# Kernel optimization log

Measured on AMD Instinct MI355X. Metric: run time of the kernel, lower is better.

The kernel has to match this reference:

```python
import jax, jax.numpy as jnp
import numpy as np

N_EMBD = 1024
N_HEAD = 16
HEAD_DIM = N_EMBD // N_HEAD


def setup_inputs() -> dict:
    key = jax.random.key(0)
    ks = jax.random.split(key, 9)
    B, T, C = 2, 2048, N_EMBD
    s = 1.0 / np.sqrt(C)
    x = jax.random.normal(ks[0], (B, T, C), dtype=jnp.float32)
    Wk = jax.random.normal(ks[1], (C, C), dtype=jnp.float32) * s
    bk = jnp.zeros((C,), dtype=jnp.float32)
    Wq = jax.random.normal(ks[2], (C, C), dtype=jnp.float32) * s
    bq = jnp.zeros((C,), dtype=jnp.float32)
    Wv = jax.random.normal(ks[3], (C, C), dtype=jnp.float32) * s
    bv = jnp.zeros((C,), dtype=jnp.float32)
    Wp = jax.random.normal(ks[4], (C, C), dtype=jnp.float32) * s
    bp = jnp.zeros((C,), dtype=jnp.float32)
    return {"x": x, "Wk": Wk, "bk": bk, "Wq": Wq, "bq": bq,
            "Wv": Wv, "bv": bv, "Wp": Wp, "bp": bp}


def reference(x, Wk, bk, Wq, bq, Wv, bv, Wp, bp):
    B, T, C = x.shape
    H, D = N_HEAD, HEAD_DIM
    # torch Linear: y = x @ W.T + b
    k = (x @ Wk.T + bk).reshape(B, T, H, D)  # [B,T,H,D]
    q = (x @ Wq.T + bq).reshape(B, T, H, D)
    v = (x @ Wv.T + bv).reshape(B, T, H, D)
    scale = 1.0 / jnp.sqrt(jnp.asarray(D, dtype=x.dtype))
    scores = jnp.einsum('bqhd,bkhd->bhqk', q, k) * scale  # [B,H,T,T]
    w = jax.nn.softmax(scores, axis=-1)
    attn = jnp.einsum('bhqk,bkhd->bqhd', w, v).reshape(B, T, C)
    return attn @ Wp.T + bp
```

## Files before the change

### kernel.cpp

```cpp
#include <hip/hip_runtime.h>
#include <hip/hip_bf16.h>
#include <stdint.h>

#define TT 2048
#define CC 1024
#define NH 16
#define HD 64
#define QKVN 3072

typedef __attribute__((ext_vector_type(8))) short short8;
typedef __attribute__((ext_vector_type(4))) float floatx4;
typedef __attribute__((ext_vector_type(4))) unsigned short ushortx4;

typedef const __attribute__((address_space(1))) void gas_void;
typedef __attribute__((address_space(3))) void las_void;

__device__ __forceinline__ void gload16(const void* g, void* l) {
  __builtin_amdgcn_global_load_lds((gas_void*)g, (las_void*)l, 16, 0, 0);
}

__device__ __forceinline__ unsigned short f2bf(float f) {
  union { float f; uint32_t u; } v; v.f = f;
  uint32_t u = v.u;
  uint32_t r = (u + 0x7fffu + ((u >> 16) & 1u)) >> 16;
  return (unsigned short)r;
}

__device__ __forceinline__ float fexp2(float x) {
#if __has_builtin(__builtin_amdgcn_exp2f)
  return __builtin_amdgcn_exp2f(x);
#else
  return exp2f(x);
#endif
}

#define QSCALE 0.18033688011112042f

__device__ __forceinline__ int perm64(int t) {
  const int kk = t >> 5, r5 = t & 31;
  const int g = ((r5 >> 3) & 2) | ((r5 >> 2) & 1);
  const int slot = (r5 & 3) | ((r5 >> 1) & 4);
  return kk * 32 + g * 8 + slot;
}

__global__ __launch_bounds__(256) void cvt_fused(const float* __restrict__ x,
                                                 const float* __restrict__ wq,
                                                 const float* __restrict__ wk,
                                                 const float* __restrict__ wv,
                                                 const float* __restrict__ wp,
                                                 unsigned short* __restrict__ xb,
                                                 unsigned short* __restrict__ wqkvb,
                                                 unsigned short* __restrict__ wpb) {
  const int i = blockIdx.x * blockDim.x + threadIdx.x;
  if (i < 1048576) {
    const float4 v = reinterpret_cast<const float4*>(x)[i];
    ushortx4 o; o[0] = f2bf(v.x); o[1] = f2bf(v.y); o[2] = f2bf(v.z); o[3] = f2bf(v.w);
    reinterpret_cast<ushortx4*>(xb)[i] = o;
    return;
  }
  const int j = i - 1048576;
  const int seg = j >> 18;
  const int idx = j & 262143;
  const float* src = (seg == 0) ? wq : (seg == 1) ? wk : (seg == 2) ? wv : wp;
  const float sc = (seg == 0) ? QSCALE : 1.0f;
  const float4 v = reinterpret_cast<const float4*>(src)[idx];
  ushortx4 o;
  o[0] = f2bf(v.x * sc); o[1] = f2bf(v.y * sc); o[2] = f2bf(v.z * sc); o[3] = f2bf(v.w * sc);
  if (seg < 3)
    reinterpret_cast<ushortx4*>(wqkvb)[j] = o;
  else
    reinterpret_cast<ushortx4*>(wpb)[idx] = o;
}

template<int OUTF32, int VOUT>
__global__ __launch_bounds__(256) void gemm_bt(const unsigned short* __restrict__ A,
                                               const unsigned short* __restrict__ W,
                                               const float* __restrict__ b0,
                                               const float* __restrict__ b1,
                                               const float* __restrict__ b2,
                                               float bs0,
                                               void* __restrict__ outv,
                                               unsigned short* __restrict__ Vt,
                                               int M, int N, int K) {
  __shared__ unsigned short lsA[128 * 64];
  __shared__ unsigned short lsB[128 * 64];
  const int tid = threadIdx.x;
  const int wave = tid >> 6, lane = tid & 63;
  const int m0 = blockIdx.y * 128, n0 = blockIdx.x * 128;
  const int wm = (wave >> 1) * 64, wn = (wave & 1) * 64;
  const float* bias = (n0 < 1024) ? b0 : (n0 < 2048 ? b1 : b2);
  const float bsc = (n0 < 1024) ? bs0 : 1.0f;

  floatx4 acc[4][4];
#pragma unroll
  for (int i = 0; i < 4; ++i)
#pragma unroll
    for (int j = 0; j < 4; ++j)
      acc[i][j] = (floatx4){0.f, 0.f, 0.f, 0.f};

  const int sr = lane >> 3;
  const int sj = lane & 7;

  for (int kt = 0; kt < K; kt += 64) {
    __syncthreads();
#pragma unroll
    for (int t = 0; t < 4; ++t) {
      const int g4 = wave * 4 + t;
      const int r = g4 * 8 + sr;
      const int gj = (sj ^ (r & 7)) << 3;
      gload16(A + (size_t)(m0 + r) * K + kt + gj, (char*)lsA + g4 * 1024);
      gload16(W + (size_t)(n0 + r) * K + kt + gj, (char*)lsB + g4 * 1024);
    }
    __syncthreads();

#pragma unroll
    for (int kk = 0; kk < 2; ++kk) {
      short8 af[4], bfr[4];
#pragma unroll
      for (int i = 0; i < 4; ++i) {
        const int ra = wm + i * 16 + (lane & 15);
        const int ca = (kk * 4 + (lane >> 4)) ^ (ra & 7);
        af[i] = *reinterpret_cast<const short8*>((const char*)lsA + ra * 128 + (ca << 4));
        const int rb = wn + i * 16 + (lane & 15);
        const int cb = (kk * 4 + (lane >> 4)) ^ (rb & 7);
        bfr[i] = *reinterpret_cast<const short8*>((const char*)lsB + rb * 128 + (cb << 4));
      }
#pragma unroll
      for (int i = 0; i < 4; ++i)
#pragma unroll
        for (int j = 0; j < 4; ++j)
          acc[i][j] = __builtin_amdgcn_mfma_f32_16x16x32_bf16(af[i], bfr[j], acc[i][j], 0, 0, 0);
    }
  }

  const int col = lane & 15;
  const int rgrp = (lane >> 4) * 4;

  if (VOUT && n0 >= 2048) {
#pragma unroll
    for (int i = 0; i < 4; ++i) {
      const int tk0 = m0 + wm + i * 16 + rgrp;
      const int bb = tk0 >> 11;
      const int tw = tk0 & 2047;
      const int tpos = (tw & ~63) + perm64(tw & 63);
#pragma unroll
      for (int j = 0; j < 4; ++j) {
        const int vdim = n0 - 2048 + wn + j * 16 + col;
        const int h = vdim >> 6, d = vdim & 63;
        const float bv = bias[vdim] * bsc;
        ushortx4 ov;
#pragma unroll
        for (int r = 0; r < 4; ++r) ov[r] = f2bf(acc[i][j][r] + bv);
        *reinterpret_cast<ushortx4*>(
            &Vt[((size_t)((bb * NH + h) * HD + d)) * TT + tpos]) = ov;
      }
    }
    return;
  }

#pragma unroll
  for (int i = 0; i < 4; ++i) {
    const int gm0 = m0 + wm + i * 16 + rgrp;
#pragma unroll
    for (int j = 0; j < 4; ++j) {
      const int gn = n0 + wn + j * 16 + col;
      const float bv = bias[gn & 1023] * bsc;
#pragma unroll
      for (int r = 0; r < 4; ++r) {
        const float v = acc[i][j][r] + bv;
        if (OUTF32)
          reinterpret_cast<float*>(outv)[(size_t)(gm0 + r) * N + gn] = v;
        else
          reinterpret_cast<unsigned short*>(outv)[(size_t)(gm0 + r) * N + gn] = f2bf(v);
      }
    }
  }
}

__global__ __launch_bounds__(256) void attn_fwd(const unsigned short* __restrict__ QKV,
                                                const unsigned short* __restrict__ Vt,
                                                unsigned short* __restrict__ Ob) {
  __shared__ unsigned short lsK[2][64 * 64];
  __shared__ unsigned short lsV[2][64 * 64];
  const int tid = threadIdx.x;
  const int wave = tid >> 6, lane = tid & 63;
  const int g = lane >> 4;
  const int c16 = lane & 15;
  const int bh = blockIdx.y;
  const int b = bh >> 4, h = bh & 15;
  const int qw = blockIdx.x * 128 + wave * 32;

  short8 qf[2][2];
#pragma unroll
  for (int qb = 0; qb < 2; ++qb) {
    const unsigned short* qp =
        QKV + (size_t)(b * TT + qw + qb * 16 + c16) * QKVN + h * HD + g * 8;
    qf[qb][0] = *reinterpret_cast<const short8*>(qp);
    qf[qb][1] = *reinterpret_cast<const short8*>(qp + 32);
  }

  short8 ones;
#pragma unroll
  for (int i = 0; i < 8; ++i) ones[i] = (short)0x3F80;

  floatx4 o[2][4];
#pragma unroll
  for (int qb = 0; qb < 2; ++qb)
#pragma unroll
    for (int f = 0; f < 4; ++f) o[qb][f] = (floatx4){0.f, 0.f, 0.f, 0.f};
  floatx4 lacc[2];
  lacc[0] = (floatx4){0.f, 0.f, 0.f, 0.f};
  lacc[1] = (floatx4){0.f, 0.f, 0.f, 0.f};

  const int sr = lane >> 3, sj = lane & 7;

  auto stage = [&](int buf, int kt) {
#pragma unroll
    for (int t = 0; t < 2; ++t) {
      const int g8 = wave * 2 + t;
      const int r = g8 * 8 + sr;
      const int gj = (sj ^ (r & 7)) << 3;
      gload16(QKV + (size_t)(b * TT + kt + r) * QKVN + CC + h * HD + gj,
              (char*)lsK[buf] + g8 * 1024);
      gload16(Vt + ((size_t)bh * HD + r) * TT + kt + gj, (char*)lsV[buf] + g8 * 1024);
    }
  };

  auto compute = [&](const unsigned short* lk, const unsigned short* lv) {
    floatx4 s[2][4];
#pragma unroll
    for (int qb = 0; qb < 2; ++qb)
#pragma unroll
      for (int cb = 0; cb < 4; ++cb) s[qb][cb] = (floatx4){0.f, 0.f, 0.f, 0.f};
    __builtin_amdgcn_s_setprio(1);
#pragma unroll
    for (int kk = 0; kk < 2; ++kk) {
#pragma unroll
      for (int cb = 0; cb < 4; ++cb) {
        const int rk = cb * 16 + c16;
        const int ck = (kk * 4 + g) ^ (rk & 7);
        const short8 kf =
            *reinterpret_cast<const short8*>((const char*)lk + rk * 128 + (ck << 4));
        s[0][cb] = __builtin_amdgcn_mfma_f32_16x16x32_bf16(kf, qf[0][kk], s[0][cb], 0, 0, 0);
        s[1][cb] = __builtin_amdgcn_mfma_f32_16x16x32_bf16(kf, qf[1][kk], s[1][cb], 0, 0, 0);
      }
    }
    __builtin_amdgcn_s_setprio(0);

    unsigned int w[2][4][2];
#pragma unroll
    for (int qb = 0; qb < 2; ++qb) {
#pragma unroll
      for (int cb = 0; cb < 4; ++cb) {
#pragma unroll
        for (int r = 0; r < 4; ++r) s[qb][cb][r] = fexp2(s[qb][cb][r]);
        asm("v_cvt_pk_bf16_f32 %0, %1, %2"
            : "=v"(w[qb][cb][0]) : "v"(s[qb][cb][0]), "v"(s[qb][cb][1]));
        asm("v_cvt_pk_bf16_f32 %0, %1, %2"
            : "=v"(w[qb][cb][1]) : "v"(s[qb][cb][2]), "v"(s[qb][cb][3]));
      }
    }

#pragma unroll
    for (int kk = 0; kk < 2; ++kk) {
      short8 pbv[2];
#pragma unroll
      for (int qb = 0; qb < 2; ++qb) {
        unsigned int pa0 = w[qb][2 * kk][0], pb0 = w[qb][2 * kk + 1][0];
        unsigned int pa1 = w[qb][2 * kk][1], pb1 = w[qb][2 * kk + 1][1];
        asm("v_permlane32_swap_b32 %0, %1" : "+v"(pa0), "+v"(pb0));
        asm("v_permlane32_swap_b32 %0, %1" : "+v"(pa1), "+v"(pb1));
        union { unsigned int u[4]; short8 v; } pk;
        pk.u[0] = pa0; pk.u[1] = pa1; pk.u[2] = pb0; pk.u[3] = pb1;
        pbv[qb] = pk.v;
      }
      __builtin_amdgcn_s_setprio(1);
#pragma unroll
      for (int f = 0; f < 4; ++f) {
        const int rv = f * 16 + c16;
        const int cv = (4 * kk + g) ^ (rv & 7);
        const short8 vf =
            *reinterpret_cast<const short8*>((const char*)lv + rv * 128 + (cv << 4));
        o[0][f] = __builtin_amdgcn_mfma_f32_16x16x32_bf16(vf, pbv[0], o[0][f], 0, 0, 0);
        o[1][f] = __builtin_amdgcn_mfma_f32_16x16x32_bf16(vf, pbv[1], o[1][f], 0, 0, 0);
      }
      lacc[0] = __builtin_amdgcn_mfma_f32_16x16x32_bf16(ones, pbv[0], lacc[0], 0, 0, 0);
      lacc[1] = __builtin_amdgcn_mfma_f32_16x16x32_bf16(ones, pbv[1], lacc[1], 0, 0, 0);
      __builtin_amdgcn_s_setprio(0);
    }
  };

  stage(0, 0);

#pragma unroll 2
  for (int it = 0; it < TT / 64; ++it) {
    const int buf = it & 1;
    if (it < TT / 64 - 1) {
      stage(buf ^ 1, (it + 1) * 64);
      asm volatile("s_waitcnt vmcnt(4)" ::: "memory");
    } else {
      asm volatile("s_waitcnt vmcnt(0)" ::: "memory");
    }
    __builtin_amdgcn_s_barrier();
    __builtin_amdgcn_sched_barrier(0);
    compute((const unsigned short*)lsK[buf], (const unsigned short*)lsV[buf]);
    __builtin_amdgcn_s_barrier();
  }

#pragma unroll
  for (int qb = 0; qb < 2; ++qb) {
    const float inv = 1.0f / lacc[qb][0];
    const size_t gm = (size_t)(b * TT + qw + qb * 16 + c16) * CC;
#pragma unroll
    for (int f = 0; f < 4; ++f) {
      ushortx4 ov;
#pragma unroll
      for (int r = 0; r < 4; ++r) ov[r] = f2bf(o[qb][f][r] * inv);
      *reinterpret_cast<ushortx4*>(&Ob[gm + h * HD + f * 16 + 4 * g]) = ov;
    }
  }
}

extern "C" void kernel_launch(void* const* d_in, const int* in_sizes, int n_in,
                              void* d_out, int out_size, void* d_ws, size_t ws_size,
                              hipStream_t stream) {
  (void)in_sizes; (void)n_in; (void)out_size; (void)ws_size;
  const float* x  = (const float*)d_in[0];
  const float* Wk = (const float*)d_in[1];
  const float* bk = (const float*)d_in[2];
  const float* Wq = (const float*)d_in[3];
  const float* bq = (const float*)d_in[4];
  const float* Wv = (const float*)d_in[5];
  const float* bv = (const float*)d_in[6];
  const float* Wp = (const float*)d_in[7];
  const float* bp = (const float*)d_in[8];
  float* out = (float*)d_out;

  char* ws = (char*)d_ws;
  const size_t MB = 1u << 20;
  unsigned short* xb    = (unsigned short*)(ws);
  unsigned short* Wqkvb = (unsigned short*)(ws + 8 * MB);
  unsigned short* Wpb   = (unsigned short*)(ws + 14 * MB);
  unsigned short* QKVb  = (unsigned short*)(ws + 16 * MB);
  unsigned short* Vtb   = (unsigned short*)(ws + 40 * MB);
  unsigned short* Ab    = (unsigned short*)(ws + 48 * MB);

  const int M = 2 * TT;

  cvt_fused<<<8192, 256, 0, stream>>>(x, Wq, Wk, Wv, Wp, xb, Wqkvb, Wpb);

  gemm_bt<0, 1><<<dim3(QKVN / 128, M / 128), 256, 0, stream>>>(
      xb, Wqkvb, bq, bk, bv, QSCALE, QKVb, Vtb, M, QKVN, CC);

  attn_fwd<<<dim3(TT / 128, 2 * NH), 256, 0, stream>>>(QKVb, Vtb, Ab);

  gemm_bt<1, 0><<<dim3(CC / 128, M / 128), 256, 0, stream>>>(
      Ab, Wpb, bp, bp, bp, 1.0f, out, nullptr, M, CC, CC);
}
```

Measured before the change: 130.0 us.

## Halve attention query tile per wave and reorder grid for more blocks

Each wave now handles 16 query rows instead of 32, so a block covers 64 queries and the grid doubles to 1024 blocks. The grid is also swapped so head/batch is the fast index, which places blocks sharing the same K/V next to each other in launch order. The intent is more parallelism and occupancy across the CUs with lower register pressure. In exchange, each block reloads every K/V tile for half as many queries, so LDS staging traffic and barrier overhead per unit of work double.

New measurement: 130.3 us. Within noise of the previous version (+0.2%).

```diff
diff --git a/kernel.cpp b/kernel.cpp
--- a/kernel.cpp
+++ b/kernel.cpp
@@ -186,31 +186,26 @@
   const int wave = tid >> 6, lane = tid & 63;
   const int g = lane >> 4;
   const int c16 = lane & 15;
-  const int bh = blockIdx.y;
+  const int bh = blockIdx.x;
   const int b = bh >> 4, h = bh & 15;
-  const int qw = blockIdx.x * 128 + wave * 32;
-
-  short8 qf[2][2];
-#pragma unroll
-  for (int qb = 0; qb < 2; ++qb) {
+  const int q0 = blockIdx.y * 64 + wave * 16;
+
+  short8 qf[2];
+  {
     const unsigned short* qp =
-        QKV + (size_t)(b * TT + qw + qb * 16 + c16) * QKVN + h * HD + g * 8;
-    qf[qb][0] = *reinterpret_cast<const short8*>(qp);
-    qf[qb][1] = *reinterpret_cast<const short8*>(qp + 32);
+        QKV + (size_t)(b * TT + q0 + c16) * QKVN + h * HD + g * 8;
+    qf[0] = *reinterpret_cast<const short8*>(qp);
+    qf[1] = *reinterpret_cast<const short8*>(qp + 32);
   }
 
   short8 ones;
 #pragma unroll
   for (int i = 0; i < 8; ++i) ones[i] = (short)0x3F80;
 
-  floatx4 o[2][4];
-#pragma unroll
-  for (int qb = 0; qb < 2; ++qb)
-#pragma unroll
-    for (int f = 0; f < 4; ++f) o[qb][f] = (floatx4){0.f, 0.f, 0.f, 0.f};
-  floatx4 lacc[2];
-  lacc[0] = (floatx4){0.f, 0.f, 0.f, 0.f};
-  lacc[1] = (floatx4){0.f, 0.f, 0.f, 0.f};
+  floatx4 o[4];
+#pragma unroll
+  for (int f = 0; f < 4; ++f) o[f] = (floatx4){0.f, 0.f, 0.f, 0.f};
+  floatx4 lacc = (floatx4){0.f, 0.f, 0.f, 0.f};
 
   const int sr = lane >> 3, sj = lane & 7;
 
@@ -227,11 +222,9 @@
   };
 
   auto compute = [&](const unsigned short* lk, const unsigned short* lv) {
-    floatx4 s[2][4];
-#pragma unroll
-    for (int qb = 0; qb < 2; ++qb)
-#pragma unroll
-      for (int cb = 0; cb < 4; ++cb) s[qb][cb] = (floatx4){0.f, 0.f, 0.f, 0.f};
+    floatx4 s[4];
+#pragma unroll
+    for (int cb = 0; cb < 4; ++cb) s[cb] = (floatx4){0.f, 0.f, 0.f, 0.f};
     __builtin_amdgcn_s_setprio(1);
 #pragma unroll
     for (int kk = 0; kk < 2; ++kk) {
@@ -241,39 +234,31 @@
         const int ck = (kk * 4 + g) ^ (rk & 7);
         const short8 kf =
             *reinterpret_cast<const short8*>((const char*)lk + rk * 128 + (ck << 4));
-        s[0][cb] = __builtin_amdgcn_mfma_f32_16x16x32_bf16(kf, qf[0][kk], s[0][cb], 0, 0, 0);
-        s[1][cb] = __builtin_amdgcn_mfma_f32_16x16x32_bf16(kf, qf[1][kk], s[1][cb], 0, 0, 0);
+        s[cb] = __builtin_amdgcn_mfma_f32_16x16x32_bf16(kf, qf[kk], s[cb], 0, 0, 0);
       }
     }
     __builtin_amdgcn_s_setprio(0);
 
-    unsigned int w[2][4][2];
-#pragma unroll
-    for (int qb = 0; qb < 2; ++qb) {
-#pragma unroll
-      for (int cb = 0; cb < 4; ++cb) {
-#pragma unroll
-        for (int r = 0; r < 4; ++r) s[qb][cb][r] = fexp2(s[qb][cb][r]);
-        asm("v_cvt_pk_bf16_f32 %0, %1, %2"
-            : "=v"(w[qb][cb][0]) : "v"(s[qb][cb][0]), "v"(s[qb][cb][1]));
-        asm("v_cvt_pk_bf16_f32 %0, %1, %2"
-            : "=v"(w[qb][cb][1]) : "v"(s[qb][cb][2]), "v"(s[qb][cb][3]));
-      }
+    unsigned int w[4][2];
+#pragma unroll
+    for (int cb = 0; cb < 4; ++cb) {
+#pragma unroll
+      for (int r = 0; r < 4; ++r) s[cb][r] = fexp2(s[cb][r]);
+      asm("v_cvt_pk_bf16_f32 %0, %1, %2"
+          : "=v"(w[cb][0]) : "v"(s[cb][0]), "v"(s[cb][1]));
+      asm("v_cvt_pk_bf16_f32 %0, %1, %2"
+          : "=v"(w[cb][1]) : "v"(s[cb][2]), "v"(s[cb][3]));
     }
 
 #pragma unroll
     for (int kk = 0; kk < 2; ++kk) {
-      short8 pbv[2];
-#pragma unroll
-      for (int qb = 0; qb < 2; ++qb) {
-        unsigned int pa0 = w[qb][2 * kk][0], pb0 = w[qb][2 * kk + 1][0];
-        unsigned int pa1 = w[qb][2 * kk][1], pb1 = w[qb][2 * kk + 1][1];
-        asm("v_permlane32_swap_b32 %0, %1" : "+v"(pa0), "+v"(pb0));
-        asm("v_permlane32_swap_b32 %0, %1" : "+v"(pa1), "+v"(pb1));
-        union { unsigned int u[4]; short8 v; } pk;
-        pk.u[0] = pa0; pk.u[1] = pa1; pk.u[2] = pb0; pk.u[3] = pb1;
-        pbv[qb] = pk.v;
-      }
+      unsigned int pa0 = w[2 * kk][0], pb0 = w[2 * kk + 1][0];
+      unsigned int pa1 = w[2 * kk][1], pb1 = w[2 * kk + 1][1];
+      asm("v_permlane32_swap_b32 %0, %1" : "+v"(pa0), "+v"(pb0));
+      asm("v_permlane32_swap_b32 %0, %1" : "+v"(pa1), "+v"(pb1));
+      union { unsigned int u[4]; short8 v; } pk;
+      pk.u[0] = pa0; pk.u[1] = pa1; pk.u[2] = pb0; pk.u[3] = pb1;
+      const short8 pbv = pk.v;
       __builtin_amdgcn_s_setprio(1);
 #pragma unroll
       for (int f = 0; f < 4; ++f) {
@@ -281,11 +266,9 @@
         const int cv = (4 * kk + g) ^ (rv & 7);
         const short8 vf =
             *reinterpret_cast<const short8*>((const char*)lv + rv * 128 + (cv << 4));
-        o[0][f] = __builtin_amdgcn_mfma_f32_16x16x32_bf16(vf, pbv[0], o[0][f], 0, 0, 0);
-        o[1][f] = __builtin_amdgcn_mfma_f32_16x16x32_bf16(vf, pbv[1], o[1][f], 0, 0, 0);
-      }
-      lacc[0] = __builtin_amdgcn_mfma_f32_16x16x32_bf16(ones, pbv[0], lacc[0], 0, 0, 0);
-      lacc[1] = __builtin_amdgcn_mfma_f32_16x16x32_bf16(ones, pbv[1], lacc[1], 0, 0, 0);
+        o[f] = __builtin_amdgcn_mfma_f32_16x16x32_bf16(vf, pbv, o[f], 0, 0, 0);
+      }
+      lacc = __builtin_amdgcn_mfma_f32_16x16x32_bf16(ones, pbv, lacc, 0, 0, 0);
       __builtin_amdgcn_s_setprio(0);
     }
   };
@@ -307,15 +290,14 @@
     __builtin_amdgcn_s_barrier();
   }
 
-#pragma unroll
-  for (int qb = 0; qb < 2; ++qb) {
-    const float inv = 1.0f / lacc[qb][0];
-    const size_t gm = (size_t)(b * TT + qw + qb * 16 + c16) * CC;
+  {
+    const float inv = 1.0f / lacc[0];
+    const size_t gm = (size_t)(b * TT + q0 + c16) * CC;
 #pragma unroll
     for (int f = 0; f < 4; ++f) {
       ushortx4 ov;
 #pragma unroll
-      for (int r = 0; r < 4; ++r) ov[r] = f2bf(o[qb][f][r] * inv);
+      for (int r = 0; r < 4; ++r) ov[r] = f2bf(o[f][r] * inv);
       *reinterpret_cast<ushortx4*>(&Ob[gm + h * HD + f * 16 + 4 * g]) = ov;
     }
   }
@@ -352,7 +334,7 @@
   gemm_bt<0, 1><<<dim3(QKVN / 128, M / 128), 256, 0, stream>>>(
       xb, Wqkvb, bq, bk, bv, QSCALE, QKVb, Vtb, M, QKVN, CC);
 
-  attn_fwd<<<dim3(TT / 128, 2 * NH), 256, 0, stream>>>(QKVb, Vtb, Ab);
+  attn_fwd<<<dim3(2 * NH, TT / 64), 256, 0, stream>>>(QKVb, Vtb, Ab);
 
   gemm_bt<1, 0><<<dim3(CC / 128, M / 128), 256, 0, stream>>>(
       Ab, Wpb, bp, bp, bp, 1.0f, out, nullptr, M, CC, CC);
```
